# Performance work log

Measured on AMD Instinct MI355X. Metric: run time of the kernel, lower is better.

The kernel has to match this reference:

```python
import jax, jax.numpy as jnp
import numpy as np

SIM_THRESHOLD = 0.8


def setup_inputs() -> dict:
    key = jax.random.key(0)
    k1, k2, k3 = jax.random.split(key, 3)
    B, K = 256, 65536
    output = jax.random.normal(k1, (B, K + 1), dtype=jnp.float32)
    # cosine similarities in [-1, 1]
    cosine_similarities = jax.random.uniform(k2, (B, K), dtype=jnp.float32,
                                             minval=-1.0, maxval=1.0)
    target = jax.random.randint(k3, (B,), 0, 1)  # unused by the loss (label hardcoded to 0)
    return {"output": output, "cosine_similarities": cosine_similarities,
            "target": target}


def reference(output, cosine_similarities, target):
    # Per sample: keep logit 0 (positive) always; keep negative j iff cos_sim < threshold.
    # CE with label 0 on the masked logits == logsumexp(kept logits) - logit_0.
    # Masking with -inf reproduces masked_select exactly for the softmax/CE math,
    # without ragged shapes or a Python loop.
    B = output.shape[0]
    keep_neg = cosine_similarities < SIM_THRESHOLD            # [B, K]
    keep = jnp.concatenate([jnp.ones((B, 1), dtype=bool), keep_neg], axis=1)  # [B, K+1]
    masked_logits = jnp.where(keep, output, -jnp.inf)
    # loss_i = -log_softmax(masked_logits)[0] = logsumexp(masked) - logit_0
    losses = jax.nn.logsumexp(masked_logits, axis=1) - output[:, 0]
    return losses.mean()
```

## Files before the change

### kernel.cpp

```cpp
#include <hip/hip_runtime.h>

#define SIM_T 0.8f

typedef float f32x4 __attribute__((ext_vector_type(4)));

__device__ __forceinline__ f32x4 ntload4(const float* p) {
  return __builtin_nontemporal_load(reinterpret_cast<const f32x4*>(p));
}
__device__ __forceinline__ float ntload1(const float* p) {
  return __builtin_nontemporal_load(p);
}

__global__ __launch_bounds__(256) void pruner_partial(
    const float* __restrict__ out, const float* __restrict__ cs,
    float* __restrict__ ws, float* __restrict__ o0s, int K, int parts) {
  const int per_part = K / parts;
  const int row  = blockIdx.x / parts;
  const int part = blockIdx.x % parts;
  const int tid  = threadIdx.x;

  const float* crow = cs  + (size_t)row * K + (size_t)part * per_part;
  const float* orow = out + (size_t)row * (K + 1) + 1 + (size_t)part * per_part;

  if (part == 0 && tid == 0) o0s[row] = orow[-1];

  float a0 = 0.f, a1 = 0.f, a2 = 0.f, a3 = 0.f;

  for (int kb = tid * 4; kb < per_part; kb += 4096) {
    f32x4 c0 = ntload4(crow + kb);
    f32x4 c1 = ntload4(crow + kb + 1024);
    f32x4 c2 = ntload4(crow + kb + 2048);
    f32x4 c3 = ntload4(crow + kb + 3072);
    float x00 = ntload1(orow + kb +    0), x01 = ntload1(orow + kb +    1);
    float x02 = ntload1(orow + kb +    2), x03 = ntload1(orow + kb +    3);
    float x10 = ntload1(orow + kb + 1024), x11 = ntload1(orow + kb + 1025);
    float x12 = ntload1(orow + kb + 1026), x13 = ntload1(orow + kb + 1027);
    float x20 = ntload1(orow + kb + 2048), x21 = ntload1(orow + kb + 2049);
    float x22 = ntload1(orow + kb + 2050), x23 = ntload1(orow + kb + 2051);
    float x30 = ntload1(orow + kb + 3072), x31 = ntload1(orow + kb + 3073);
    float x32 = ntload1(orow + kb + 3074), x33 = ntload1(orow + kb + 3075);
    a0 += (c0.x < SIM_T) ? __expf(x00) : 0.f;
    a1 += (c0.y < SIM_T) ? __expf(x01) : 0.f;
    a2 += (c0.z < SIM_T) ? __expf(x02) : 0.f;
    a3 += (c0.w < SIM_T) ? __expf(x03) : 0.f;
    a0 += (c1.x < SIM_T) ? __expf(x10) : 0.f;
    a1 += (c1.y < SIM_T) ? __expf(x11) : 0.f;
    a2 += (c1.z < SIM_T) ? __expf(x12) : 0.f;
    a3 += (c1.w < SIM_T) ? __expf(x13) : 0.f;
    a0 += (c2.x < SIM_T) ? __expf(x20) : 0.f;
    a1 += (c2.y < SIM_T) ? __expf(x21) : 0.f;
    a2 += (c2.z < SIM_T) ? __expf(x22) : 0.f;
    a3 += (c2.w < SIM_T) ? __expf(x23) : 0.f;
    a0 += (c3.x < SIM_T) ? __expf(x30) : 0.f;
    a1 += (c3.y < SIM_T) ? __expf(x31) : 0.f;
    a2 += (c3.z < SIM_T) ? __expf(x32) : 0.f;
    a3 += (c3.w < SIM_T) ? __expf(x33) : 0.f;
  }
  float s = (a0 + a1) + (a2 + a3);

#pragma unroll
  for (int off = 32; off > 0; off >>= 1) s += __shfl_down(s, off, 64);

  __shared__ float lds[4];
  if ((tid & 63) == 0) lds[tid >> 6] = s;
  __syncthreads();
  if (tid == 0) ws[blockIdx.x] = (lds[0] + lds[1]) + (lds[2] + lds[3]);
}

__global__ __launch_bounds__(256) void pruner_partial_simple(
    const float* __restrict__ out, const float* __restrict__ cs,
    float* __restrict__ ws, float* __restrict__ o0s, int K, int parts) {
  const int per_part = K / parts;
  const int row  = blockIdx.x / parts;
  const int part = blockIdx.x % parts;
  const int tid  = threadIdx.x;
  const float* crow = cs  + (size_t)row * K + (size_t)part * per_part;
  const float* orow = out + (size_t)row * (K + 1) + 1 + (size_t)part * per_part;
  if (part == 0 && tid == 0) o0s[row] = orow[-1];
  float a = 0.f;
  for (int k = tid; k < per_part; k += 256)
    a += (crow[k] < SIM_T) ? __expf(orow[k]) : 0.f;
#pragma unroll
  for (int off = 32; off > 0; off >>= 1) a += __shfl_down(a, off, 64);
  __shared__ float lds[4];
  if ((tid & 63) == 0) lds[tid >> 6] = a;
  __syncthreads();
  if (tid == 0) ws[blockIdx.x] = (lds[0] + lds[1]) + (lds[2] + lds[3]);
}

__global__ __launch_bounds__(256) void pruner_final(
    const float* __restrict__ ws, const float* __restrict__ o0s,
    float* __restrict__ res, int parts, int B) {
  const int i = threadIdx.x;
  float loss = 0.0f;
  if (i < B) {
    float t = 0.0f;
    for (int p = 0; p < parts; ++p) t += ws[i * parts + p];
    const float o0 = o0s[i];
    t += __expf(o0);
    loss = logf(t) - o0;
  }
#pragma unroll
  for (int off = 32; off > 0; off >>= 1) loss += __shfl_down(loss, off, 64);
  __shared__ float lds[4];
  if ((i & 63) == 0) lds[i >> 6] = loss;
  __syncthreads();
  if (i == 0) res[0] = ((lds[0] + lds[1]) + (lds[2] + lds[3])) / (float)B;
}

extern "C" void kernel_launch(void* const* d_in, const int* in_sizes, int n_in,
                              void* d_out, int out_size, void* d_ws, size_t ws_size,
                              hipStream_t stream) {
  const float* out = (const float*)d_in[0];
  const float* cs  = (const float*)d_in[1];
  float* res = (float*)d_out;

  const int B = in_sizes[2];
  const int K = in_sizes[1] / B;

  const int PARTS = 8;
  float* ws  = (float*)d_ws;
  float* o0s = ws + (size_t)B * PARTS;

  if ((K / PARTS) % 4096 == 0) {
    pruner_partial<<<B * PARTS, 256, 0, stream>>>(out, cs, ws, o0s, K, PARTS);
  } else {
    pruner_partial_simple<<<B * PARTS, 256, 0, stream>>>(out, cs, ws, o0s, K, PARTS);
  }
  pruner_final<<<1, 256, 0, stream>>>(ws, o0s, res, PARTS, B);
}
```

Measured before the change: 26.20 us.

## Use one 1024-thread block per row and fuse final reduction via atomicAdd

Replaces the 8-part-per-row partial kernel plus a separate final kernel with one 1024-thread block per row. Each block computes its row's loss and atomically adds the loss scaled by 1/B into the result, which is zeroed by a memset. This removes the second kernel launch and the workspace round-trip. In exchange the grid shrinks to 256 blocks, which may under-occupy the GPU, and the floating-point atomics make the summation order nondeterministic.

```diff
diff --git a/kernel.cpp b/kernel.cpp
--- a/kernel.cpp
+++ b/kernel.cpp
@@ -11,34 +11,30 @@
   return __builtin_nontemporal_load(p);
 }
 
-__global__ __launch_bounds__(256) void pruner_partial(
+__global__ __launch_bounds__(1024) void pruner_row(
     const float* __restrict__ out, const float* __restrict__ cs,
-    float* __restrict__ ws, float* __restrict__ o0s, int K, int parts) {
-  const int per_part = K / parts;
-  const int row  = blockIdx.x / parts;
-  const int part = blockIdx.x % parts;
-  const int tid  = threadIdx.x;
+    float* __restrict__ res, int K, float invB) {
+  const int row = blockIdx.x;
+  const int tid = threadIdx.x;
 
-  const float* crow = cs  + (size_t)row * K + (size_t)part * per_part;
-  const float* orow = out + (size_t)row * (K + 1) + 1 + (size_t)part * per_part;
-
-  if (part == 0 && tid == 0) o0s[row] = orow[-1];
+  const float* crow = cs  + (size_t)row * K;
+  const float* orow = out + (size_t)row * (K + 1) + 1;
 
   float a0 = 0.f, a1 = 0.f, a2 = 0.f, a3 = 0.f;
 
-  for (int kb = tid * 4; kb < per_part; kb += 4096) {
+  for (int kb = tid * 4; kb < K; kb += 16384) {
     f32x4 c0 = ntload4(crow + kb);
-    f32x4 c1 = ntload4(crow + kb + 1024);
-    f32x4 c2 = ntload4(crow + kb + 2048);
-    f32x4 c3 = ntload4(crow + kb + 3072);
-    float x00 = ntload1(orow + kb +    0), x01 = ntload1(orow + kb +    1);
-    float x02 = ntload1(orow + kb +    2), x03 = ntload1(orow + kb +    3);
-    float x10 = ntload1(orow + kb + 1024), x11 = ntload1(orow + kb + 1025);
-    float x12 = ntload1(orow + kb + 1026), x13 = ntload1(orow + kb + 1027);
-    float x20 = ntload1(orow + kb + 2048), x21 = ntload1(orow + kb + 2049);
-    float x22 = ntload1(orow + kb + 2050), x23 = ntload1(orow + kb + 2051);
-    float x30 = ntload1(orow + kb + 3072), x31 = ntload1(orow + kb + 3073);
-    float x32 = ntload1(orow + kb + 3074), x33 = ntload1(orow + kb + 3075);
+    f32x4 c1 = ntload4(crow + kb + 4096);
+    f32x4 c2 = ntload4(crow + kb + 8192);
+    f32x4 c3 = ntload4(crow + kb + 12288);
+    float x00 = ntload1(orow + kb +     0), x01 = ntload1(orow + kb +     1);
+    float x02 = ntload1(orow + kb +     2), x03 = ntload1(orow + kb +     3);
+    float x10 = ntload1(orow + kb +  4096), x11 = ntload1(orow + kb +  4097);
+    float x12 = ntload1(orow + kb +  4098), x13 = ntload1(orow + kb +  4099);
+    float x20 = ntload1(orow + kb +  8192), x21 = ntload1(orow + kb +  8193);
+    float x22 = ntload1(orow + kb +  8194), x23 = ntload1(orow + kb +  8195);
+    float x30 = ntload1(orow + kb + 12288), x31 = ntload1(orow + kb + 12289);
+    float x32 = ntload1(orow + kb + 12290), x33 = ntload1(orow + kb + 12291);
     a0 += (c0.x < SIM_T) ? __expf(x00) : 0.f;
     a1 += (c0.y < SIM_T) ? __expf(x01) : 0.f;
     a2 += (c0.z < SIM_T) ? __expf(x02) : 0.f;
@@ -61,10 +57,23 @@
 #pragma unroll
   for (int off = 32; off > 0; off >>= 1) s += __shfl_down(s, off, 64);
 
-  __shared__ float lds[4];
+  __shared__ float lds[16];
   if ((tid & 63) == 0) lds[tid >> 6] = s;
   __syncthreads();
-  if (tid == 0) ws[blockIdx.x] = (lds[0] + lds[1]) + (lds[2] + lds[3]);
+
+  if (tid == 0) {
+    float t0 = 0.f, t1 = 0.f, t2 = 0.f, t3 = 0.f;
+#pragma unroll
+    for (int w = 0; w < 16; w += 4) {
+      t0 += lds[w + 0];
+      t1 += lds[w + 1];
+      t2 += lds[w + 2];
+      t3 += lds[w + 3];
+    }
+    const float o0 = orow[-1];
+    const float t = (t0 + t1) + (t2 + t3) + __expf(o0);
+    atomicAdd(res, (logf(t) - o0) * invB);
+  }
 }
 
 __global__ __launch_bounds__(256) void pruner_partial_simple(
@@ -118,14 +127,14 @@
   const int B = in_sizes[2];
   const int K = in_sizes[1] / B;
 
-  const int PARTS = 8;
-  float* ws  = (float*)d_ws;
-  float* o0s = ws + (size_t)B * PARTS;
-
-  if ((K / PARTS) % 4096 == 0) {
-    pruner_partial<<<B * PARTS, 256, 0, stream>>>(out, cs, ws, o0s, K, PARTS);
+  if (K % 16384 == 0) {
+    hipMemsetAsync(res, 0, sizeof(float), stream);
+    pruner_row<<<B, 1024, 0, stream>>>(out, cs, res, K, 1.0f / (float)B);
   } else {
+    const int PARTS = 8;
+    float* ws  = (float*)d_ws;
+    float* o0s = ws + (size_t)B * PARTS;
     pruner_partial_simple<<<B * PARTS, 256, 0, stream>>>(out, cs, ws, o0s, K, PARTS);
+    pruner_final<<<1, 256, 0, stream>>>(ws, o0s, res, PARTS, B);
   }
-  pruner_final<<<1, 256, 0, stream>>>(ws, o0s, res, PARTS, B);
 }
```

Result: slower. 30.97 us (+18.2%).
